# Optimization experiments

Hardware: AMD Instinct MI355X
Metric: run time of the kernel (lower is better)

The kernel has to match this reference:

```python
import jax, jax.numpy as jnp
import numpy as np

NNZ = 819200
VOCAB = 1000000
EMBED = 64
BATCH = 4096


def setup_inputs() -> dict:
    key = jax.random.key(0)
    k1, k2, k3, k4 = jax.random.split(key, 4)
    feature_embedding = jax.random.normal(k1, (VOCAB, EMBED), dtype=jnp.float32) * 0.05
    feature_vals = jax.random.uniform(k2, (NNZ,), dtype=jnp.float32)
    batch_ids = jnp.sort(jax.random.randint(k3, (NNZ,), 0, BATCH, dtype=jnp.int32))
    feat_ids = jax.random.randint(k4, (NNZ,), 0, VOCAB, dtype=jnp.int32)
    return {
        "feature_embedding": feature_embedding,
        "feature_vals": feature_vals,
        "batch_ids": batch_ids,
        "feat_ids": feat_ids,
        "batch_size": BATCH,
    }


def reference(feature_embedding, feature_vals, batch_ids, feat_ids, batch_size):
    # Gather embedding rows for each nonzero (sparse_dense_matmul == gather + segment_sum)
    emb = feature_embedding[feat_ids]                      # [nnz, D]
    v = feature_vals[:, None]                              # [nnz, 1]
    # sum over features per batch row of v * e, then square
    s = jax.ops.segment_sum(v * emb, batch_ids, num_segments=batch_size)       # [B, D]
    sum_square = s * s
    # sum over features per batch row of v^2 * e^2
    square_sum = jax.ops.segment_sum((v * v) * (emb * emb), batch_ids,
                                     num_segments=batch_size)                   # [B, D]
    return 0.5 * (sum_square - square_sum)
```

## Files before the change

kernel.cpp:

```cpp
#include <hip/hip_runtime.h>

#define EMBED 64
#define BATCH 4096
#define G     8

__global__ __launch_bounds__(256) void seg_bounds(
    const int* __restrict__ bids, int* __restrict__ start,
    int* __restrict__ end_, int nnz)
{
    int i = blockIdx.x * blockDim.x + threadIdx.x;
    if (i >= nnz) return;
    int b = bids[i];
    if (i == 0 || bids[i - 1] != b) start[b] = i;
    if (i == nnz - 1 || bids[i + 1] != b) end_[b] = i + 1;
}

__global__ __launch_bounds__(256) void fm_row(
    const float4* __restrict__ emb4,
    const float*  __restrict__ vals,
    const int*    __restrict__ fids,
    const int*    __restrict__ start,
    const int*    __restrict__ end_,
    float4*       __restrict__ out4)
{
    const int wave = (blockIdx.x * blockDim.x + threadIdx.x) >> 6;
    const int lane = threadIdx.x & 63;
    const int grp  = lane >> 4;
    const int sub  = lane & 15;
    const int r    = wave;
    if (r >= BATCH) return;

    const int s0 = start[r];
    if (s0 < 0) {
        if (grp == 0) out4[r * 16 + sub] = make_float4(0.f, 0.f, 0.f, 0.f);
        return;
    }
    const int s1 = end_[r];

    int   idx   = s0 + lane;
    int   f_cur = fids[min(idx, s1 - 1)];
    float v_cur = (idx < s1) ? vals[idx] : 0.f;

    float4 s = make_float4(0.f, 0.f, 0.f, 0.f);
    float4 q = make_float4(0.f, 0.f, 0.f, 0.f);

    for (int w0 = s0; w0 < s1; w0 += 64) {
        int nbase = w0 + 64;
        int f_nxt = 0; float v_nxt = 0.f;
        if (nbase < s1) {
            int nidx = nbase + lane;
            int c    = min(nidx, s1 - 1);
            f_nxt = fids[c];
            v_nxt = (nidx < s1) ? vals[nidx] : 0.f;
        }
        const int lim = min(64, s1 - w0);
        #pragma unroll
        for (int b = 0; b < 2; ++b) {
            if (b * 32 >= lim) break;
            float4 e[G]; float vv[G];
            #pragma unroll
            for (int g = 0; g < G; ++g) {
                int j  = b * 32 + 4 * g + grp;
                int f  = __shfl(f_cur, j);
                vv[g]  = __shfl(v_cur, j);
                e[g]   = emb4[(size_t)f * 16 + sub];
            }
            #pragma unroll
            for (int g = 0; g < G; ++g) {
                float ax = vv[g] * e[g].x, ay = vv[g] * e[g].y;
                float az = vv[g] * e[g].z, aw = vv[g] * e[g].w;
                s.x += ax;      s.y += ay;      s.z += az;      s.w += aw;
                q.x += ax * ax; q.y += ay * ay; q.z += az * az; q.w += aw * aw;
            }
        }
        f_cur = f_nxt; v_cur = v_nxt;
    }

    #pragma unroll
    for (int m = 16; m <= 32; m <<= 1) {
        s.x += __shfl_xor(s.x, m); s.y += __shfl_xor(s.y, m);
        s.z += __shfl_xor(s.z, m); s.w += __shfl_xor(s.w, m);
        q.x += __shfl_xor(q.x, m); q.y += __shfl_xor(q.y, m);
        q.z += __shfl_xor(q.z, m); q.w += __shfl_xor(q.w, m);
    }
    if (grp == 0) {
        float4 o;
        o.x = 0.5f * (s.x * s.x - q.x);
        o.y = 0.5f * (s.y * s.y - q.y);
        o.z = 0.5f * (s.z * s.z - q.z);
        o.w = 0.5f * (s.w * s.w - q.w);
        out4[r * 16 + sub] = o;
    }
}

extern "C" void kernel_launch(void* const* d_in, const int* in_sizes, int n_in,
                              void* d_out, int out_size, void* d_ws, size_t ws_size,
                              hipStream_t stream) {
    const float4* emb4 = (const float4*)d_in[0];
    const float*  vals = (const float*)d_in[1];
    const int*    bids = (const int*)d_in[2];
    const int*    fids = (const int*)d_in[3];
    float4*       out4 = (float4*)d_out;
    const int nnz = in_sizes[1];

    int* start = (int*)d_ws;
    int* end_  = start + BATCH;

    hipMemsetAsync(start, 0xFF, BATCH * sizeof(int), stream);

    seg_bounds<<<dim3((nnz + 255) / 256), dim3(256), 0, stream>>>(
        bids, start, end_, nnz);

    const int blocks = BATCH / 4;
    fm_row<<<dim3(blocks), dim3(256), 0, stream>>>(
        emb4, vals, fids, start, end_, out4);
}
```

Baseline: 335.0 us.

## Split each batch row across four waves and replace memset with lower-bound offsets

Each batch row now gets a whole 256-thread block, and its four waves stride over the row's nonzeros and combine their partial sums through shared memory. The start/end arrays and the memset are replaced by one lower-bound offset array that also covers empty rows. The aim is four times more waves in flight for the latency-bound embedding gather, at the cost of a block-level sync and dropping the next-chunk index prefetch. Launch bounds now request a minimum occupancy as well.

New measurement: 332.9 us. No clear change (-0.6%).

```diff
diff --git a/kernel.cpp b/kernel.cpp
--- a/kernel.cpp
+++ b/kernel.cpp
@@ -4,55 +4,42 @@
 #define BATCH 4096
 #define G     8
 
-__global__ __launch_bounds__(256) void seg_bounds(
-    const int* __restrict__ bids, int* __restrict__ start,
-    int* __restrict__ end_, int nnz)
+__global__ __launch_bounds__(256) void seg_lb(
+    const int* __restrict__ bids, int* __restrict__ lb, int nnz)
 {
     int i = blockIdx.x * blockDim.x + threadIdx.x;
     if (i >= nnz) return;
-    int b = bids[i];
-    if (i == 0 || bids[i - 1] != b) start[b] = i;
-    if (i == nnz - 1 || bids[i + 1] != b) end_[b] = i + 1;
+    int b  = bids[i];
+    int bp = (i == 0) ? -1 : bids[i - 1];
+    for (int r = bp + 1; r <= b; ++r) lb[r] = i;
+    if (i == nnz - 1)
+        for (int r = b + 1; r <= BATCH; ++r) lb[r] = nnz;
 }
 
-__global__ __launch_bounds__(256) void fm_row(
+__global__ __launch_bounds__(256, 6) void fm_row(
     const float4* __restrict__ emb4,
     const float*  __restrict__ vals,
     const int*    __restrict__ fids,
-    const int*    __restrict__ start,
-    const int*    __restrict__ end_,
+    const int*    __restrict__ lb,
     float4*       __restrict__ out4)
 {
-    const int wave = (blockIdx.x * blockDim.x + threadIdx.x) >> 6;
+    const int r    = blockIdx.x;
+    const int wv   = threadIdx.x >> 6;
     const int lane = threadIdx.x & 63;
     const int grp  = lane >> 4;
     const int sub  = lane & 15;
-    const int r    = wave;
-    if (r >= BATCH) return;
 
-    const int s0 = start[r];
-    if (s0 < 0) {
-        if (grp == 0) out4[r * 16 + sub] = make_float4(0.f, 0.f, 0.f, 0.f);
-        return;
-    }
-    const int s1 = end_[r];
-
-    int   idx   = s0 + lane;
-    int   f_cur = fids[min(idx, s1 - 1)];
-    float v_cur = (idx < s1) ? vals[idx] : 0.f;
+    const int s0 = lb[r];
+    const int s1 = lb[r + 1];
 
     float4 s = make_float4(0.f, 0.f, 0.f, 0.f);
     float4 q = make_float4(0.f, 0.f, 0.f, 0.f);
 
-    for (int w0 = s0; w0 < s1; w0 += 64) {
-        int nbase = w0 + 64;
-        int f_nxt = 0; float v_nxt = 0.f;
-        if (nbase < s1) {
-            int nidx = nbase + lane;
-            int c    = min(nidx, s1 - 1);
-            f_nxt = fids[c];
-            v_nxt = (nidx < s1) ? vals[nidx] : 0.f;
-        }
+    for (int w0 = s0 + (wv << 6); w0 < s1; w0 += 4 * 64) {
+        int   idx   = w0 + lane;
+        int   c     = min(idx, s1 - 1);
+        int   f_cur = fids[c];
+        float v_cur = (idx < s1) ? vals[idx] : 0.f;
         const int lim = min(64, s1 - w0);
         #pragma unroll
         for (int b = 0; b < 2; ++b) {
@@ -73,7 +60,6 @@
                 q.x += ax * ax; q.y += ay * ay; q.z += az * az; q.w += aw * aw;
             }
         }
-        f_cur = f_nxt; v_cur = v_nxt;
     }
 
     #pragma unroll
@@ -83,13 +69,24 @@
         q.x += __shfl_xor(q.x, m); q.y += __shfl_xor(q.y, m);
         q.z += __shfl_xor(q.z, m); q.w += __shfl_xor(q.w, m);
     }
-    if (grp == 0) {
+
+    __shared__ float4 sb[4][16], qb[4][16];
+    if (grp == 0) { sb[wv][sub] = s; qb[wv][sub] = q; }
+    __syncthreads();
+    if (threadIdx.x < 16) {
+        float4 S = sb[0][lane], Q = qb[0][lane];
+        #pragma unroll
+        for (int w = 1; w < 4; ++w) {
+            float4 a = sb[w][lane], c2 = qb[w][lane];
+            S.x += a.x;  S.y += a.y;  S.z += a.z;  S.w += a.w;
+            Q.x += c2.x; Q.y += c2.y; Q.z += c2.z; Q.w += c2.w;
+        }
         float4 o;
-        o.x = 0.5f * (s.x * s.x - q.x);
-        o.y = 0.5f * (s.y * s.y - q.y);
-        o.z = 0.5f * (s.z * s.z - q.z);
-        o.w = 0.5f * (s.w * s.w - q.w);
-        out4[r * 16 + sub] = o;
+        o.x = 0.5f * (S.x * S.x - Q.x);
+        o.y = 0.5f * (S.y * S.y - Q.y);
+        o.z = 0.5f * (S.z * S.z - Q.z);
+        o.w = 0.5f * (S.w * S.w - Q.w);
+        out4[r * 16 + lane] = o;
     }
 }
 
@@ -103,15 +100,10 @@
     float4*       out4 = (float4*)d_out;
     const int nnz = in_sizes[1];
 
-    int* start = (int*)d_ws;
-    int* end_  = start + BATCH;
+    int* lb = (int*)d_ws;
 
-    hipMemsetAsync(start, 0xFF, BATCH * sizeof(int), stream);
+    seg_lb<<<dim3((nnz + 255) / 256), dim3(256), 0, stream>>>(bids, lb, nnz);
 
-    seg_bounds<<<dim3((nnz + 255) / 256), dim3(256), 0, stream>>>(
-        bids, start, end_, nnz);
-
-    const int blocks = BATCH / 4;
-    fm_row<<<dim3(blocks), dim3(256), 0, stream>>>(
-        emb4, vals, fids, start, end_, out4);
+    fm_row<<<dim3(BATCH), dim3(256), 0, stream>>>(
+        emb4, vals, fids, lb, out4);
 }
```
